# Kernel tuning notes

Measured on AMD Instinct MI355X. Metric: run time of the kernel, lower is better.

## Reference

```python
import jax, jax.numpy as jnp
import numpy as np

H, W = 16, 16  # input_resolution
NUM_HEADS = 16
DIM = 512


def build_relative_position_index(h, w):
    coords = np.stack(np.meshgrid(np.arange(h), np.arange(w), indexing='ij'))  # [2,h,w]
    cf = coords.reshape(2, -1)
    rel = cf[:, :, None] - cf[:, None, :]            # [2,N,N]
    rel = rel.transpose(1, 2, 0).astype(np.int32)    # [N,N,2]
    rel[:, :, 0] += h - 1
    rel[:, :, 1] += w - 1
    rel[:, :, 0] *= 2 * w - 1
    return jnp.asarray(rel.sum(-1).reshape(-1), dtype=jnp.int32)  # [N*N]


def setup_inputs() -> dict:
    key = jax.random.key(0)
    ks = jax.random.split(key, 6)
    B, N, C = 128, H * W, DIM
    x = jax.random.normal(ks[0], (B, N, C), dtype=jnp.float32)
    qkv_w = jax.random.normal(ks[1], (3 * C, C), dtype=jnp.float32) * (C ** -0.5)
    qkv_b = jax.random.normal(ks[2], (3 * C,), dtype=jnp.float32) * 0.02
    proj_w = jax.random.normal(ks[3], (C, C), dtype=jnp.float32) * (C ** -0.5)
    proj_b = jax.random.normal(ks[4], (C,), dtype=jnp.float32) * 0.02
    bias_table = jax.random.normal(ks[5], ((2 * H - 1) * (2 * W - 1), NUM_HEADS), dtype=jnp.float32) * 0.02
    rel_index = build_relative_position_index(H, W)
    return {"x": x, "qkv_w": qkv_w, "qkv_b": qkv_b, "proj_w": proj_w,
            "proj_b": proj_b, "bias_table": bias_table, "rel_index": rel_index}


def reference(x, qkv_w, qkv_b, proj_w, proj_b, bias_table, rel_index):
    B, N, C = x.shape
    h = NUM_HEADS
    hd = C // h
    scale = hd ** -0.5
    # qkv projection: [B,N,3C] -> [3,B,h,N,hd]
    qkv = (jnp.einsum('bnc,oc->bno', x, qkv_w) + qkv_b)
    qkv = qkv.reshape(B, N, 3, h, hd).transpose(2, 0, 3, 1, 4)
    q, k, v = qkv[0], qkv[1], qkv[2]
    # relative position bias: gather [N*N,h] -> [1,h,N,N]
    bias = bias_table[rel_index].reshape(N, N, h).transpose(2, 0, 1)[None]
    attn = jnp.einsum('bhnd,bhmd->bhnm', q * scale, k) + bias
    attn = jax.nn.softmax(attn, axis=-1)
    out = jnp.einsum('bhnm,bhmd->bhnd', attn, v)     # [B,h,N,hd]
    out = out.transpose(0, 2, 1, 3).reshape(B, N, C)
    return jnp.einsum('bnc,oc->bno', out, proj_w) + proj_b
```

## Files before the change

kernel.cpp:

```cpp
#include <hip/hip_runtime.h>

typedef __bf16 bf16_t;
typedef __bf16 bf16x8 __attribute__((ext_vector_type(8)));
typedef float f32x4 __attribute__((ext_vector_type(4)));

#define MFMA_16x16x32(a, b, c) __builtin_amdgcn_mfma_f32_16x16x32_bf16((a), (b), (c), 0, 0, 0)

__device__ inline bf16x8 cvt8(const float* __restrict__ p) {
  bf16x8 r;
#pragma unroll
  for (int j = 0; j < 8; j++) r[j] = (bf16_t)p[j];
  return r;
}

__device__ inline void load_lds16(const bf16_t* g, bf16_t* l) {
  __builtin_amdgcn_global_load_lds(
      (const __attribute__((address_space(1))) void*)g,
      (__attribute__((address_space(3))) void*)l, 16, 0, 0);
}

__global__ __launch_bounds__(256) void convert_k(
    const float* __restrict__ x, const float* __restrict__ qkv_w,
    const float* __restrict__ proj_w,
    bf16_t* __restrict__ xbf, bf16_t* __restrict__ wqkvbf,
    bf16_t* __restrict__ wprojbf) {
  size_t base = ((size_t)blockIdx.x * 256 + threadIdx.x) * 8;
  if (base < 16777216) {
    *(bf16x8*)(xbf + base) = cvt8(x + base);
  } else if (base < 17563648) {
    size_t o = base - 16777216;
    *(bf16x8*)(wqkvbf + o) = cvt8(qkv_w + o);
  } else {
    size_t o = base - 17563648;
    *(bf16x8*)(wprojbf + o) = cvt8(proj_w + o);
  }
}

__global__ __launch_bounds__(256) void bias_gather_k(
    const float* __restrict__ table, const int* __restrict__ rel,
    float* __restrict__ biasws) {
  int idx = blockIdx.x * 256 + threadIdx.x;
  int h = idx >> 16;
  int rem = idx & 65535;
  int rb = rem >> 12;
  int ct = (rem >> 8) & 15;
  int L = (rem >> 2) & 63;
  int r = idx & 3;
  int row = rb * 16 + (L >> 4) * 4 + r;
  int col = ct * 16 + (L & 15);
  biasws[idx] = table[rel[row * 256 + col] * 16 + h];
}

#define PH_MID()                                          \
  do {                                                    \
    __builtin_amdgcn_s_barrier();                         \
    asm volatile("s_waitcnt lgkmcnt(0)" ::: "memory");    \
    __builtin_amdgcn_sched_barrier(0);                    \
    __builtin_amdgcn_s_setprio(1);                        \
  } while (0)

#define PH_END()                                          \
  do {                                                    \
    __builtin_amdgcn_s_setprio(0);                        \
    __builtin_amdgcn_s_barrier();                         \
    __builtin_amdgcn_sched_barrier(0);                    \
  } while (0)

#define STG_A2(buf, g, c)                                                        \
  do {                                                                           \
    load_lds16(ga + ((g)&7) * 64 + (c)*32768, la + (buf)*16384 + (c)*4096);      \
    load_lds16(ga + ((g)&7) * 64 + ((c) + 1) * 32768,                            \
               la + (buf)*16384 + ((c) + 1) * 4096);                             \
  } while (0)
#define STG_B2(buf, g, c)                                                        \
  do {                                                                           \
    load_lds16(gb + ((g) >> 3) * 131072 + ((g)&7) * 64 + (c)*32768,              \
               lb + (buf)*16384 + (c)*4096);                                     \
    load_lds16(gb + ((g) >> 3) * 131072 + ((g)&7) * 64 + ((c) + 1) * 32768,      \
               lb + (buf)*16384 + ((c) + 1) * 4096);                             \
  } while (0)

#define RDA(dst, buf, ibase)                                                     \
  _Pragma("unroll") for (int i = 0; i < 4; ++i) {                                \
    dst[i][0] = *(const bf16x8*)&As[(buf)*16384 + a0 + ((ibase) + i) * 1024];    \
    dst[i][1] = *(const bf16x8*)&As[(buf)*16384 + a1 + ((ibase) + i) * 1024];    \
  }
#define RDB(dst, buf, jbase)                                                     \
  _Pragma("unroll") for (int j = 0; j < 2; ++j) {                                \
    dst[j][0] = *(const bf16x8*)&Bs[(buf)*16384 + b0 + ((jbase) + j) * 1024];    \
    dst[j][1] = *(const bf16x8*)&Bs[(buf)*16384 + b1 + ((jbase) + j) * 1024];    \
  }

#define MFQ(Af, Bf, I0, J0)                                                      \
  _Pragma("unroll") for (int i = 0; i < 4; ++i) _Pragma("unroll")                \
      for (int j = 0; j < 2; ++j) {                                              \
    acc[(I0) + i][(J0) + j] =                                                    \
        MFMA_16x16x32(Af[i][0], Bf[j][0], acc[(I0) + i][(J0) + j]);              \
    acc[(I0) + i][(J0) + j] =                                                    \
        MFMA_16x16x32(Af[i][1], Bf[j][1], acc[(I0) + i][(J0) + j]);              \
  }

#define GROUP(G, NT)                                                             \
  do {                                                                           \
    {                                                                            \
      bf16x8 fal[4][2], fbl[2][2], fah[4][2], fbh[2][2];                         \
      RDA(fal, 0, 0); RDB(fbl, 0, 0);                                            \
      if ((2 * (G) + 1) < (NT)) STG_B2(1, 2 * (G) + 1, 0);                       \
      PH_MID(); MFQ(fal, fbl, 0, 0); PH_END();                                   \
      RDA(fah, 0, 4);                                                            \
      if ((2 * (G) + 1) < (NT)) STG_B2(1, 2 * (G) + 1, 2);                       \
      PH_MID(); MFQ(fah, fbl, 4, 0); PH_END();                                   \
      RDB(fbh, 0, 2);                                                            \
      if ((2 * (G) + 2) < (NT)) STG_A2(0, 2 * (G) + 2, 0);                       \
      PH_MID(); MFQ(fah, fbh, 4, 2); PH_END();                                   \
      if ((2 * (G) + 2) < (NT)) STG_A2(0, 2 * (G) + 2, 2);                       \
      PH_MID(); MFQ(fal, fbh, 0, 2);                                             \
      __builtin_amdgcn_s_setprio(0);                                             \
      if ((2 * (G) + 2) < (NT))                                                  \
        asm volatile("s_waitcnt vmcnt(4)" ::: "memory");                         \
      else                                                                       \
        asm volatile("s_waitcnt vmcnt(0)" ::: "memory");                         \
      __builtin_amdgcn_s_barrier();                                              \
      __builtin_amdgcn_sched_barrier(0);                                         \
    }                                                                            \
    {                                                                            \
      bf16x8 fal[4][2], fbl[2][2], fah[4][2], fbh[2][2];                         \
      RDA(fal, 1, 0); RDB(fbl, 1, 0);                                            \
      if ((2 * (G) + 2) < (NT)) STG_B2(0, 2 * (G) + 2, 0);                       \
      PH_MID(); MFQ(fal, fbl, 0, 0); PH_END();                                   \
      RDA(fah, 1, 4);                                                            \
      if ((2 * (G) + 2) < (NT)) STG_B2(0, 2 * (G) + 2, 2);                       \
      PH_MID(); MFQ(fah, fbl, 4, 0); PH_END();                                   \
      RDB(fbh, 1, 2);                                                            \
      if ((2 * (G) + 3) < (NT)) STG_A2(1, 2 * (G) + 3, 0);                       \
      PH_MID(); MFQ(fah, fbh, 4, 2); PH_END();                                   \
      if ((2 * (G) + 3) < (NT)) STG_A2(1, 2 * (G) + 3, 2);                       \
      PH_MID(); MFQ(fal, fbh, 0, 2);                                             \
      __builtin_amdgcn_s_setprio(0);                                             \
      if ((2 * (G) + 3) < (NT))                                                  \
        asm volatile("s_waitcnt vmcnt(4)" ::: "memory");                         \
      else                                                                       \
        asm volatile("s_waitcnt vmcnt(0)" ::: "memory");                         \
      __builtin_amdgcn_s_barrier();                                              \
      __builtin_amdgcn_sched_barrier(0);                                         \
    }                                                                            \
  } while (0)

#define GEMM_SETUP(Ap, Wp)                                                       \
  __shared__ bf16_t As[2 * 16384];                                               \
  __shared__ bf16_t Bs[2 * 16384];                                               \
  const int t = threadIdx.x;                                                     \
  const int w = t >> 6, L = t & 63;                                              \
  const int wm = w >> 2, wn = w & 3;                                             \
  const int lrow = L & 15, lq = L >> 4;                                          \
  const int srow = t >> 3;                                                       \
  const int sslot = (t & 7) ^ (srow & 7);                                        \
  const bf16_t* ga = (Ap) + (size_t)(m0 + srow) * 512 + sslot * 8;               \
  const bf16_t* gb = (Wp) + (size_t)(n0 + srow) * 512 + sslot * 8;               \
  bf16_t* la = As + t * 8;                                                       \
  bf16_t* lb = Bs + t * 8;                                                       \
  const int m8 = (lrow & 7) * 8;                                                 \
  const int a0 = (wm * 128 + lrow) * 64 + ((lq * 8) ^ m8);                       \
  const int a1 = (wm * 128 + lrow) * 64 + ((32 + lq * 8) ^ m8);                  \
  const int b0 = (wn * 64 + lrow) * 64 + ((lq * 8) ^ m8);                        \
  const int b1 = (wn * 64 + lrow) * 64 + ((32 + lq * 8) ^ m8);

#define PROLOGUE()                                                               \
  STG_A2(0, 0, 0); STG_A2(0, 0, 2);                                              \
  STG_B2(0, 0, 0); STG_B2(0, 0, 2);                                              \
  STG_A2(1, 1, 0); STG_A2(1, 1, 2);                                              \
  asm volatile("s_waitcnt vmcnt(4)" ::: "memory");                               \
  __builtin_amdgcn_s_barrier();                                                  \
  __builtin_amdgcn_sched_barrier(0);

__global__ __launch_bounds__(512, 2) void qkv_gemm256_k(
    const bf16_t* __restrict__ A, const bf16_t* __restrict__ W,
    const float* __restrict__ Bvec,
    bf16_t* __restrict__ qws, bf16_t* __restrict__ kws, bf16_t* __restrict__ vws) {
  const int id = blockIdx.x;
  const int lin = (id & 7) * 32 + (id >> 3);
  const int mt = lin >> 1;
  const int ntb = (lin & 1) * 3;
  const int m0 = mt * 256;
  const int n0 = ntb * 256;

  GEMM_SETUP(A, W);

  float bias_r[3][4];
#pragma unroll
  for (int ot = 0; ot < 3; ++ot) {
    int c0 = (ntb + ot) * 256 + wn * 64;
#pragma unroll
    for (int jj = 0; jj < 4; ++jj) bias_r[ot][jj] = Bvec[c0 + jj * 16 + lrow];
  }

  f32x4 acc[8][4];
#pragma unroll
  for (int i = 0; i < 8; ++i)
#pragma unroll
    for (int jj = 0; jj < 4; ++jj) {
      float bv = bias_r[0][jj];
      acc[i][jj] = (f32x4){bv, bv, bv, bv};
    }

  PROLOGUE();

#pragma unroll
  for (int G = 0; G < 12; ++G) {
    GROUP(G, 24);
    if ((G & 3) == 3) {
      const int ot = G >> 2;
      const int col0 = (ntb + ot) * 256 + wn * 64;
      const int s = col0 >> 9;
      bf16_t* dst = (s == 0) ? qws : (s == 1) ? kws : vws;
      const float mul = (s == 0) ? 0.17677669529663687f : 1.0f;
#pragma unroll
      for (int jj = 0; jj < 4; ++jj) {
        int o = col0 + jj * 16 + lrow;
        int rem = o & 511;
        int hh = rem >> 5, d = rem & 31;
#pragma unroll
        for (int i = 0; i < 8; ++i) {
#pragma unroll
          for (int r = 0; r < 4; ++r) {
            int m = m0 + wm * 128 + i * 16 + lq * 4 + r;
            int b = m >> 8, n = m & 255;
            dst[(size_t)(((b * 16 + hh) * 256 + n) << 5) + d] =
                (bf16_t)(acc[i][jj][r] * mul);
          }
        }
      }
      if (ot < 2) {
#pragma unroll
        for (int i = 0; i < 8; ++i)
#pragma unroll
          for (int jj = 0; jj < 4; ++jj) {
            float bv = bias_r[ot + 1][jj];
            acc[i][jj] = (f32x4){bv, bv, bv, bv};
          }
      }
    }
  }
}

__global__ __launch_bounds__(512, 2) void proj_gemm256_k(
    const bf16_t* __restrict__ A, const bf16_t* __restrict__ W,
    const float* __restrict__ Bvec, float* __restrict__ out) {
  const int id = blockIdx.x;
  const int lin = (id & 7) * 32 + (id >> 3);
  const int mt = lin >> 1, nt = lin & 1;
  const int m0 = mt * 256, n0 = nt * 256;

  GEMM_SETUP(A, W);

  float bias_r[4];
#pragma unroll
  for (int jj = 0; jj < 4; ++jj)
    bias_r[jj] = Bvec[n0 + wn * 64 + jj * 16 + lrow];

  f32x4 acc[8][4];
#pragma unroll
  for (int i = 0; i < 8; ++i)
#pragma unroll
    for (int jj = 0; jj < 4; ++jj) {
      float bv = bias_r[jj];
      acc[i][jj] = (f32x4){bv, bv, bv, bv};
    }

  PROLOGUE();

#pragma unroll
  for (int G = 0; G < 4; ++G) GROUP(G, 8);

#pragma unroll
  for (int jj = 0; jj < 4; ++jj) {
    int o = n0 + wn * 64 + jj * 16 + lrow;
#pragma unroll
    for (int i = 0; i < 8; ++i) {
#pragma unroll
      for (int r = 0; r < 4; ++r) {
        int m = m0 + wm * 128 + i * 16 + lq * 4 + r;
        out[(size_t)m * 512 + o] = acc[i][jj][r];
      }
    }
  }
}

__global__ __launch_bounds__(256) void attn_k(
    const bf16_t* __restrict__ qws, const bf16_t* __restrict__ kws,
    const bf16_t* __restrict__ vws, const float* __restrict__ biasws,
    bf16_t* __restrict__ aows) {
  __shared__ __align__(16) char smem[33792 + 16896];
  bf16_t* Ps = (bf16_t*)smem;
  bf16_t* Vs = (bf16_t*)(smem + 33792);

  const int id = blockIdx.x;
  const int xcd = id & 7;
  const int jj = id >> 3;
  const int bh = (jj >> 2) * 8 + xcd;
  const int strip = jj & 3;
  const int h = bh & 15, b = bh >> 4;

  const int t = threadIdx.x;
  const int w = t >> 6, L = t & 63;
  const int lrow = L & 15, lq = L >> 4;

  const bf16_t* kbase = kws + (size_t)bh * 8192;
  const bf16_t* vbase = vws + (size_t)bh * 8192;
#pragma unroll
  for (int c = 0; c < 4; c++) {
    bf16x8 vv = *(const bf16x8*)(vbase + t * 32 + c * 8);
#pragma unroll
    for (int j = 0; j < 8; j++) Vs[(c * 8 + j) * 264 + t] = vv[j];
  }

  const bf16_t* qbase = qws + (size_t)bh * 8192 + (strip * 64 + w * 16) * 32;
  bf16x8 qf = *(const bf16x8*)(qbase + lrow * 32 + lq * 8);
  bf16x8 kf[16];
#pragma unroll
  for (int ct = 0; ct < 16; ct++)
    kf[ct] = *(const bf16x8*)(kbase + (ct * 16 + lrow) * 32 + lq * 8);

  const float* bb = biasws + h * 65536 + (strip * 4 + w) * 4096;
  f32x4 S[16];
#pragma unroll
  for (int ct = 0; ct < 16; ct++) {
    f32x4 bi = *(const f32x4*)(bb + ct * 256 + L * 4);
    S[ct] = MFMA_16x16x32(qf, kf[ct], bi);
  }

  float sm[4] = {0.f, 0.f, 0.f, 0.f};
#pragma unroll
  for (int ct = 0; ct < 16; ct++)
#pragma unroll
    for (int r = 0; r < 4; r++) {
      float e = __expf(S[ct][r]);
      S[ct][r] = e;
      sm[r] += e;
    }
#pragma unroll
  for (int r = 0; r < 4; r++)
#pragma unroll
    for (int msk = 1; msk < 16; msk <<= 1)
      sm[r] += __shfl_xor(sm[r], msk, 64);
  float inv[4];
#pragma unroll
  for (int r = 0; r < 4; r++) inv[r] = 1.0f / sm[r];

  bf16_t* Pw = Ps + w * 4224;
#pragma unroll
  for (int ct = 0; ct < 16; ct++)
#pragma unroll
    for (int r = 0; r < 4; r++)
      Pw[(lq * 4 + r) * 264 + ct * 16 + lrow] = (bf16_t)S[ct][r];

  __syncthreads();

  f32x4 O0 = {}, O1 = {};
#pragma unroll
  for (int c = 0; c < 8; c++) {
    bf16x8 pf = *(const bf16x8*)&Pw[lrow * 264 + c * 32 + lq * 8];
    bf16x8 v0 = *(const bf16x8*)&Vs[lrow * 264 + c * 32 + lq * 8];
    bf16x8 v1 = *(const bf16x8*)&Vs[(16 + lrow) * 264 + c * 32 + lq * 8];
    O0 = MFMA_16x16x32(pf, v0, O0);
    O1 = MFMA_16x16x32(pf, v1, O1);
  }
  bf16_t* obase = aows + (size_t)(b * 256 + strip * 64 + w * 16) * 512 + h * 32;
#pragma unroll
  for (int r = 0; r < 4; r++) {
    int rl = lq * 4 + r;
    obase[rl * 512 + lrow] = (bf16_t)(O0[r] * inv[r]);
    obase[rl * 512 + 16 + lrow] = (bf16_t)(O1[r] * inv[r]);
  }
}

extern "C" void kernel_launch(void* const* d_in, const int* in_sizes, int n_in,
                              void* d_out, int out_size, void* d_ws, size_t ws_size,
                              hipStream_t stream) {
  (void)in_sizes; (void)n_in; (void)out_size; (void)ws_size;
  const float* x      = (const float*)d_in[0];
  const float* qkv_w  = (const float*)d_in[1];
  const float* qkv_b  = (const float*)d_in[2];
  const float* proj_w = (const float*)d_in[3];
  const float* proj_b = (const float*)d_in[4];
  const float* table  = (const float*)d_in[5];
  const int*   rel    = (const int*)d_in[6];

  const size_t QKV_ELEMS = 16777216;
  bf16_t* qws     = (bf16_t*)d_ws;
  bf16_t* kws     = qws + QKV_ELEMS;
  bf16_t* vws     = kws + QKV_ELEMS;
  float*  biasws  = (float*)(vws + QKV_ELEMS);
  bf16_t* wqkvbf  = (bf16_t*)(biasws + 1048576);
  bf16_t* wprojbf = wqkvbf + 786432;
  bf16_t* xbf     = wprojbf + 262144;
  bf16_t* aows    = xbf;
  float*  out     = (float*)d_out;

  convert_k<<<8704, 256, 0, stream>>>(x, qkv_w, proj_w, xbf, wqkvbf, wprojbf);
  bias_gather_k<<<4096, 256, 0, stream>>>(table, rel, biasws);
  qkv_gemm256_k<<<256, 512, 0, stream>>>(xbf, wqkvbf, qkv_b, qws, kws, vws);
  attn_k<<<8192, 256, 0, stream>>>(qws, kws, vws, biasws, aows);
  proj_gemm256_k<<<256, 512, 0, stream>>>(aows, wprojbf, proj_b, out);
}
```

Before: 314.1 us.

## Split QKV GEMM into one output tile per block and share a rolled GEMM loop

```diff
diff --git a/kernel.cpp b/kernel.cpp
--- a/kernel.cpp
+++ b/kernel.cpp
@@ -66,18 +66,26 @@
     __builtin_amdgcn_sched_barrier(0);                    \
   } while (0)
 
-#define STG_A2(buf, g, c)                                                        \
+#define GATE4()                                           \
+  do {                                                    \
+    __builtin_amdgcn_s_setprio(0);                        \
+    asm volatile("s_waitcnt vmcnt(4)" ::: "memory");      \
+    __builtin_amdgcn_s_barrier();                         \
+    __builtin_amdgcn_sched_barrier(0);                    \
+  } while (0)
+
+#define GATE0()                                           \
+  do {                                                    \
+    __builtin_amdgcn_s_setprio(0);                        \
+    asm volatile("s_waitcnt vmcnt(0)" ::: "memory");      \
+    __builtin_amdgcn_s_barrier();                         \
+    __builtin_amdgcn_sched_barrier(0);                    \
+  } while (0)
+
+#define STG2(src, dst, c)                                                        \
   do {                                                                           \
-    load_lds16(ga + ((g)&7) * 64 + (c)*32768, la + (buf)*16384 + (c)*4096);      \
-    load_lds16(ga + ((g)&7) * 64 + ((c) + 1) * 32768,                            \
-               la + (buf)*16384 + ((c) + 1) * 4096);                             \
-  } while (0)
-#define STG_B2(buf, g, c)                                                        \
-  do {                                                                           \
-    load_lds16(gb + ((g) >> 3) * 131072 + ((g)&7) * 64 + (c)*32768,              \
-               lb + (buf)*16384 + (c)*4096);                                     \
-    load_lds16(gb + ((g) >> 3) * 131072 + ((g)&7) * 64 + ((c) + 1) * 32768,      \
-               lb + (buf)*16384 + ((c) + 1) * 4096);                             \
+    load_lds16((src) + (c)*32768, (dst) + (c)*4096);                             \
+    load_lds16((src) + ((c) + 1) * 32768, (dst) + ((c) + 1) * 4096);             \
   } while (0)
 
 #define RDA(dst, buf, ibase)                                                     \
@@ -99,52 +107,6 @@
     acc[(I0) + i][(J0) + j] =                                                    \
         MFMA_16x16x32(Af[i][1], Bf[j][1], acc[(I0) + i][(J0) + j]);              \
   }
-
-#define GROUP(G, NT)                                                             \
-  do {                                                                           \
-    {                                                                            \
-      bf16x8 fal[4][2], fbl[2][2], fah[4][2], fbh[2][2];                         \
-      RDA(fal, 0, 0); RDB(fbl, 0, 0);                                            \
-      if ((2 * (G) + 1) < (NT)) STG_B2(1, 2 * (G) + 1, 0);                       \
-      PH_MID(); MFQ(fal, fbl, 0, 0); PH_END();                                   \
-      RDA(fah, 0, 4);                                                            \
-      if ((2 * (G) + 1) < (NT)) STG_B2(1, 2 * (G) + 1, 2);                       \
-      PH_MID(); MFQ(fah, fbl, 4, 0); PH_END();                                   \
-      RDB(fbh, 0, 2);                                                            \
-      if ((2 * (G) + 2) < (NT)) STG_A2(0, 2 * (G) + 2, 0);                       \
-      PH_MID(); MFQ(fah, fbh, 4, 2); PH_END();                                   \
-      if ((2 * (G) + 2) < (NT)) STG_A2(0, 2 * (G) + 2, 2);                       \
-      PH_MID(); MFQ(fal, fbh, 0, 2);                                             \
-      __builtin_amdgcn_s_setprio(0);                                             \
-      if ((2 * (G) + 2) < (NT))                                                  \
-        asm volatile("s_waitcnt vmcnt(4)" ::: "memory");                         \
-      else                                                                       \
-        asm volatile("s_waitcnt vmcnt(0)" ::: "memory");                         \
-      __builtin_amdgcn_s_barrier();                                              \
-      __builtin_amdgcn_sched_barrier(0);                                         \
-    }                                                                            \
-    {                                                                            \
-      bf16x8 fal[4][2], fbl[2][2], fah[4][2], fbh[2][2];                         \
-      RDA(fal, 1, 0); RDB(fbl, 1, 0);                                            \
-      if ((2 * (G) + 2) < (NT)) STG_B2(0, 2 * (G) + 2, 0);                       \
-      PH_MID(); MFQ(fal, fbl, 0, 0); PH_END();                                   \
-      RDA(fah, 1, 4);                                                            \
-      if ((2 * (G) + 2) < (NT)) STG_B2(0, 2 * (G) + 2, 2);                       \
-      PH_MID(); MFQ(fah, fbl, 4, 0); PH_END();                                   \
-      RDB(fbh, 1, 2);                                                            \
-      if ((2 * (G) + 3) < (NT)) STG_A2(1, 2 * (G) + 3, 0);                       \
-      PH_MID(); MFQ(fah, fbh, 4, 2); PH_END();                                   \
-      if ((2 * (G) + 3) < (NT)) STG_A2(1, 2 * (G) + 3, 2);                       \
-      PH_MID(); MFQ(fal, fbh, 0, 2);                                             \
-      __builtin_amdgcn_s_setprio(0);                                             \
-      if ((2 * (G) + 3) < (NT))                                                  \
-        asm volatile("s_waitcnt vmcnt(4)" ::: "memory");                         \
-      else                                                                       \
-        asm volatile("s_waitcnt vmcnt(0)" ::: "memory");                         \
-      __builtin_amdgcn_s_barrier();                                              \
-      __builtin_amdgcn_sched_barrier(0);                                         \
-    }                                                                            \
-  } while (0)
 
 #define GEMM_SETUP(Ap, Wp)                                                       \
   __shared__ bf16_t As[2 * 16384];                                               \
@@ -166,78 +128,115 @@
   const int b1 = (wn * 64 + lrow) * 64 + ((32 + lq * 8) ^ m8);
 
 #define PROLOGUE()                                                               \
-  STG_A2(0, 0, 0); STG_A2(0, 0, 2);                                              \
-  STG_B2(0, 0, 0); STG_B2(0, 0, 2);                                              \
-  STG_A2(1, 1, 0); STG_A2(1, 1, 2);                                              \
+  STG2(ga, la, 0); STG2(ga, la, 2);                                              \
+  STG2(gb, lb, 0); STG2(gb, lb, 2);                                              \
+  STG2(ga + 64, la + 16384, 0); STG2(ga + 64, la + 16384, 2);                    \
   asm volatile("s_waitcnt vmcnt(4)" ::: "memory");                               \
   __builtin_amdgcn_s_barrier();                                                  \
   __builtin_amdgcn_sched_barrier(0);
+
+#define GEMM_LOOP()                                                              \
+  {                                                                              \
+    const bf16_t* gA = ga + 128;                                       \
+    const bf16_t* gB = gb + 64;                                        \
+    _Pragma("unroll 1") for (int G = 0; G < 3; ++G) {                            \
+      {                                                                          \
+        bf16x8 fal[4][2], fbl[2][2], fah[4][2], fbh[2][2];                       \
+        RDA(fal, 0, 0); RDB(fbl, 0, 0);                                          \
+        STG2(gB, lb + 16384, 0);                                                 \
+        PH_MID(); MFQ(fal, fbl, 0, 0); PH_END();                                 \
+        RDA(fah, 0, 4);                                                          \
+        STG2(gB, lb + 16384, 2);                                                 \
+        PH_MID(); MFQ(fah, fbl, 4, 0); PH_END();                                 \
+        RDB(fbh, 0, 2);                                                          \
+        STG2(gA, la, 0);                                                         \
+        PH_MID(); MFQ(fah, fbh, 4, 2); PH_END();                                 \
+        STG2(gA, la, 2);                                                         \
+        PH_MID(); MFQ(fal, fbh, 0, 2); GATE4();                                  \
+      }                                                                          \
+      {                                                                          \
+        bf16x8 fal[4][2], fbl[2][2], fah[4][2], fbh[2][2];                       \
+        RDA(fal, 1, 0); RDB(fbl, 1, 0);                                          \
+        STG2(gB + 64, lb, 0);                                                    \
+        PH_MID(); MFQ(fal, fbl, 0, 0); PH_END();                                 \
+        RDA(fah, 1, 4);                                                          \
+        STG2(gB + 64, lb, 2);                                                    \
+        PH_MID(); MFQ(fah, fbl, 4, 0); PH_END();                                 \
+        RDB(fbh, 1, 2);                                                          \
+        STG2(gA + 64, la + 16384, 0);                                            \
+        PH_MID(); MFQ(fah, fbh, 4, 2); PH_END();                                 \
+        STG2(gA + 64, la + 16384, 2);                                            \
+        PH_MID(); MFQ(fal, fbh, 0, 2); GATE4();                                  \
+      }                                                                          \
+      gA += 128; gB += 128;                                                      \
+    }                                                                            \
+    {                \
+      {                                                                          \
+        bf16x8 fal[4][2], fbl[2][2], fah[4][2], fbh[2][2];                       \
+        RDA(fal, 0, 0); RDB(fbl, 0, 0);                                          \
+        STG2(gB, lb + 16384, 0);                                                 \
+        PH_MID(); MFQ(fal, fbl, 0, 0); PH_END();                                 \
+        RDA(fah, 0, 4);                                                          \
+        STG2(gB, lb + 16384, 2);                                                 \
+        PH_MID(); MFQ(fah, fbl, 4, 0); PH_END();                                 \
+        RDB(fbh, 0, 2);                                                          \
+        PH_MID(); MFQ(fah, fbh, 4, 2); PH_END();                                 \
+        PH_MID(); MFQ(fal, fbh, 0, 2); GATE0();                                  \
+      }                                                                          \
+      {                                                                          \
+        bf16x8 fal[4][2], fbl[2][2], fah[4][2], fbh[2][2];                       \
+        RDA(fal, 1, 0); RDB(fbl, 1, 0);                                          \
+        PH_MID(); MFQ(fal, fbl, 0, 0); PH_END();                                 \
+        RDA(fah, 1, 4);                                                          \
+        PH_MID(); MFQ(fah, fbl, 4, 0); PH_END();                                 \
+        RDB(fbh, 1, 2);                                                          \
+        PH_MID(); MFQ(fah, fbh, 4, 2); PH_END();                                 \
+        PH_MID(); MFQ(fal, fbh, 0, 2);                                           \
+        __builtin_amdgcn_s_setprio(0);                                           \
+        __builtin_amdgcn_sched_barrier(0);                                       \
+      }                                                                          \
+    }                                                                            \
+  }
 
 __global__ __launch_bounds__(512, 2) void qkv_gemm256_k(
     const bf16_t* __restrict__ A, const bf16_t* __restrict__ W,
     const float* __restrict__ Bvec,
     bf16_t* __restrict__ qws, bf16_t* __restrict__ kws, bf16_t* __restrict__ vws) {
   const int id = blockIdx.x;
-  const int lin = (id & 7) * 32 + (id >> 3);
-  const int mt = lin >> 1;
-  const int ntb = (lin & 1) * 3;
-  const int m0 = mt * 256;
-  const int n0 = ntb * 256;
+  const int wg = (id & 7) * 96 + (id >> 3);
+  const int mt = wg / 6, nt = wg % 6;
+  const int m0 = mt * 256, n0 = nt * 256;
 
   GEMM_SETUP(A, W);
 
-  float bias_r[3][4];
-#pragma unroll
-  for (int ot = 0; ot < 3; ++ot) {
-    int c0 = (ntb + ot) * 256 + wn * 64;
-#pragma unroll
-    for (int jj = 0; jj < 4; ++jj) bias_r[ot][jj] = Bvec[c0 + jj * 16 + lrow];
-  }
-
   f32x4 acc[8][4];
 #pragma unroll
-  for (int i = 0; i < 8; ++i)
-#pragma unroll
-    for (int jj = 0; jj < 4; ++jj) {
-      float bv = bias_r[0][jj];
-      acc[i][jj] = (f32x4){bv, bv, bv, bv};
-    }
+  for (int jj = 0; jj < 4; ++jj) {
+    float bv = Bvec[n0 + wn * 64 + jj * 16 + lrow];
+#pragma unroll
+    for (int i = 0; i < 8; ++i) acc[i][jj] = (f32x4){bv, bv, bv, bv};
+  }
 
   PROLOGUE();
-
-#pragma unroll
-  for (int G = 0; G < 12; ++G) {
-    GROUP(G, 24);
-    if ((G & 3) == 3) {
-      const int ot = G >> 2;
-      const int col0 = (ntb + ot) * 256 + wn * 64;
-      const int s = col0 >> 9;
-      bf16_t* dst = (s == 0) ? qws : (s == 1) ? kws : vws;
-      const float mul = (s == 0) ? 0.17677669529663687f : 1.0f;
-#pragma unroll
-      for (int jj = 0; jj < 4; ++jj) {
-        int o = col0 + jj * 16 + lrow;
-        int rem = o & 511;
-        int hh = rem >> 5, d = rem & 31;
-#pragma unroll
-        for (int i = 0; i < 8; ++i) {
-#pragma unroll
-          for (int r = 0; r < 4; ++r) {
-            int m = m0 + wm * 128 + i * 16 + lq * 4 + r;
-            int b = m >> 8, n = m & 255;
-            dst[(size_t)(((b * 16 + hh) * 256 + n) << 5) + d] =
-                (bf16_t)(acc[i][jj][r] * mul);
-          }
-        }
-      }
-      if (ot < 2) {
-#pragma unroll
-        for (int i = 0; i < 8; ++i)
-#pragma unroll
-          for (int jj = 0; jj < 4; ++jj) {
-            float bv = bias_r[ot + 1][jj];
-            acc[i][jj] = (f32x4){bv, bv, bv, bv};
-          }
+  GEMM_LOOP();
+
+  const int col0 = n0 + wn * 64;
+  const int s = col0 >> 9;
+  bf16_t* dst = (s == 0) ? qws : (s == 1) ? kws : vws;
+  const float mul = (s == 0) ? 0.17677669529663687f : 1.0f;
+#pragma unroll
+  for (int jj = 0; jj < 4; ++jj) {
+    int o = col0 + jj * 16 + lrow;
+    int rem = o & 511;
+    int hh = rem >> 5, d = rem & 31;
+#pragma unroll
+    for (int i = 0; i < 8; ++i) {
+#pragma unroll
+      for (int r = 0; r < 4; ++r) {
+        int m = m0 + wm * 128 + i * 16 + lq * 4 + r;
+        int b = m >> 8, n = m & 255;
+        dst[(size_t)(((b * 16 + hh) * 256 + n) << 5) + d] =
+            (bf16_t)(acc[i][jj][r] * mul);
       }
     }
   }
@@ -253,24 +252,16 @@
 
   GEMM_SETUP(A, W);
 
-  float bias_r[4];
-#pragma unroll
-  for (int jj = 0; jj < 4; ++jj)
-    bias_r[jj] = Bvec[n0 + wn * 64 + jj * 16 + lrow];
-
   f32x4 acc[8][4];
 #pragma unroll
-  for (int i = 0; i < 8; ++i)
-#pragma unroll
-    for (int jj = 0; jj < 4; ++jj) {
-      float bv = bias_r[jj];
-      acc[i][jj] = (f32x4){bv, bv, bv, bv};
-    }
+  for (int jj = 0; jj < 4; ++jj) {
+    float bv = Bvec[n0 + wn * 64 + jj * 16 + lrow];
+#pragma unroll
+    for (int i = 0; i < 8; ++i) acc[i][jj] = (f32x4){bv, bv, bv, bv};
+  }
 
   PROLOGUE();
-
-#pragma unroll
-  for (int G = 0; G < 4; ++G) GROUP(G, 8);
+  GEMM_LOOP();
 
 #pragma unroll
   for (int jj = 0; jj < 4; ++jj) {
@@ -399,7 +390,7 @@
 
   convert_k<<<8704, 256, 0, stream>>>(x, qkv_w, proj_w, xbf, wqkvbf, wprojbf);
   bias_gather_k<<<4096, 256, 0, stream>>>(table, rel, biasws);
-  qkv_gemm256_k<<<256, 512, 0, stream>>>(xbf, wqkvbf, qkv_b, qws, kws, vws);
+  qkv_gemm256_k<<<768, 512, 0, stream>>>(xbf, wqkvbf, qkv_b, qws, kws, vws);
   attn_k<<<8192, 256, 0, stream>>>(qws, kws, vws, biasws, aows);
   proj_gemm256_k<<<256, 512, 0, stream>>>(aows, wprojbf, proj_b, out);
 }
```

Result: faster. 288.4 us (-8.2%).
